# Optimization experiments

Measured on AMD Instinct MI355X. Metric: run time of the kernel, lower is better.

The kernel has to match this reference:

```python
import jax, jax.numpy as jnp
import numpy as np

NEG_INF = -1000000000.0
B, N, D, H, L, DFF = 4, 1024, 512, 8, 6, 2048
DH = D // H
R2 = 10.0 ** 2  # locality_radius^2
EPS = 1e-5


def setup_inputs() -> dict:
    key = jax.random.key(0)
    ks = jax.random.split(key, 16)
    s = 0.02
    inp = {
        "tokens": jax.random.normal(ks[0], (B, N, D), jnp.float32),
        "xy": jax.random.uniform(ks[1], (B, N, 2), jnp.float32) * 100.0,
        "Wq": jax.random.normal(ks[2], (L, D, D), jnp.float32) * s,
        "Wk": jax.random.normal(ks[3], (L, D, D), jnp.float32) * s,
        "Wv": jax.random.normal(ks[4], (L, D, D), jnp.float32) * s,
        "Wo": jax.random.normal(ks[5], (L, D, D), jnp.float32) * s,
        "bo": jnp.zeros((L, D), jnp.float32),
        "W1": jax.random.normal(ks[6], (L, D, DFF), jnp.float32) * s,
        "b1": jnp.zeros((L, DFF), jnp.float32),
        "W2": jax.random.normal(ks[7], (L, DFF, D), jnp.float32) * s,
        "b2": jnp.zeros((L, D), jnp.float32),
        "g1": jnp.ones((L, D), jnp.float32),
        "be1": jnp.zeros((L, D), jnp.float32),
        "g2": jnp.ones((L, D), jnp.float32),
        "be2": jnp.zeros((L, D), jnp.float32),
        "gf": jnp.ones((D,), jnp.float32),
        "bf": jnp.zeros((D,), jnp.float32),
        "alive": jax.random.randint(ks[8], (B, N), 0, 2, dtype=jnp.int32),
        "species": jax.random.randint(ks[9], (B, N), 0, 3, dtype=jnp.int32),
        "n_agents": 512,
    }
    return inp


def _ln(x, g, b):
    m = jnp.mean(x, axis=-1, keepdims=True)
    v = jnp.mean((x - m) ** 2, axis=-1, keepdims=True)
    return (x - m) * jax.lax.rsqrt(v + EPS) * g + b


def _build_bias(alive, xy, species, dtype):
    # (B,1,N,N) additive bias, broadcast over heads (original repeats per head)
    af = alive.astype(dtype)
    bias = (1.0 - af)[:, None, None, :] * NEG_INF  # dead keys
    d2 = jnp.sum((xy[:, :, None, :] - xy[:, None, :, :]) ** 2, axis=-1)  # (B,N,N)
    bias = bias + jnp.where(d2 > R2, NEG_INF, 0.0)[:, None, :, :]
    ia = species < 2
    ip = species == 2
    ct = (ia[:, :, None] & ip[:, None, :]) | (ip[:, :, None] & ia[:, None, :])
    bias = bias + jnp.where(ct, NEG_INF, 0.0)[:, None, :, :]
    return bias


def reference(tokens, xy, Wq, Wk, Wv, Wo, bo, W1, b1, W2, b2,
              g1, be1, g2, be2, gf, bf, alive, species, n_agents):
    bias = _build_bias(alive, xy, species, tokens.dtype)
    scale = np.float32(np.sqrt(DH))
    x = tokens
    for l in range(L):
        h = _ln(x, g1[l], be1[l])
        q = (h @ Wq[l]).reshape(B, N, H, DH)
        k = (h @ Wk[l]).reshape(B, N, H, DH)
        v = (h @ Wv[l]).reshape(B, N, H, DH)
        scores = jnp.einsum('bihd,bjhd->bhij', q, k) / scale + bias
        w = jax.nn.softmax(scores, axis=-1)
        o = jnp.einsum('bhij,bjhd->bihd', w, v).reshape(B, N, D)
        x = x + (o @ Wo[l] + bo[l])
        h2 = _ln(x, g2[l], be2[l])
        ff = jax.nn.gelu(h2 @ W1[l] + b1[l], approximate=False) @ W2[l] + b2[l]
        x = x + ff
    return _ln(x, gf, bf)
```

## Files before the change

kernel.cpp:

```cpp
#include <hip/hip_runtime.h>
#include <math.h>

namespace {

constexpr int B = 4, N = 1024, D = 512, H = 8, DHd = 64, L = 6, DFFd = 2048;
constexpr int M = B * N;
constexpr int QKVS = 3 * D;
constexpr float NEG = -1000000000.0f;
constexpr float R2c = 100.0f;

typedef __attribute__((ext_vector_type(8))) short bf16x8;
typedef __attribute__((ext_vector_type(4))) float f32x4;
typedef __attribute__((ext_vector_type(16))) float f32x16;

__device__ __forceinline__ short f2bf(float f) {
  union { float f; unsigned u; } c; c.f = f;
  unsigned r = (c.u + 0x7fffu + ((c.u >> 16) & 1u)) >> 16;
  return (short)r;
}

__device__ __forceinline__ float gelu_f(float x) {
  return 0.5f * x * (1.0f + erff(x * 0.70710678118654752f));
}

__global__ __launch_bounds__(256) void bias_kernel(
    const float* __restrict__ xy, const int* __restrict__ alive,
    const int* __restrict__ species, float* __restrict__ bias)
{
  int j = blockIdx.x * 256 + threadIdx.x;
  int i = blockIdx.y;
  int b = blockIdx.z;
  float xi = xy[((size_t)b * N + i) * 2 + 0];
  float yi = xy[((size_t)b * N + i) * 2 + 1];
  float xj = xy[((size_t)b * N + j) * 2 + 0];
  float yj = xy[((size_t)b * N + j) * 2 + 1];
  float dx = xi - xj, dy = yi - yj;
  float d2 = dx * dx + dy * dy;
  float bv = 0.0f;
  if (alive[b * N + j] == 0) bv += NEG;
  if (d2 > R2c) bv += NEG;
  int si = species[b * N + i], sj = species[b * N + j];
  bool ia = si < 2, ip = si == 2, ja = sj < 2, jp = sj == 2;
  if ((ia && jp) || (ip && ja)) bv += NEG;
  bias[((size_t)b * N + i) * N + j] = bv;
}

__global__ __launch_bounds__(256) void wprep_kernel(
    const float* __restrict__ src, short* __restrict__ dst,
    int K, int Nc, size_t srcLS, size_t dstLS)
{
  __shared__ float t[32][33];
  int k0 = blockIdx.x * 32, n0 = blockIdx.y * 32;
  src += (size_t)blockIdx.z * srcLS;
  dst += (size_t)blockIdx.z * dstLS;
  int r = threadIdx.x >> 5, c = threadIdx.x & 31;
#pragma unroll
  for (int i = 0; i < 4; ++i)
    t[r + i * 8][c] = src[(size_t)(k0 + r + i * 8) * Nc + n0 + c];
  __syncthreads();
#pragma unroll
  for (int i = 0; i < 4; ++i)
    dst[(size_t)(n0 + r + i * 8) * K + k0 + c] = f2bf(t[c][r + i * 8]);
}

__global__ __launch_bounds__(64) void ln_kernel(
    const float* __restrict__ x, const float* __restrict__ g,
    const float* __restrict__ be, float* __restrict__ outf,
    short* __restrict__ outb)
{
  int row = blockIdx.x;
  int tid = threadIdx.x;
  const float* xr = x + (size_t)row * D;
  float v[8];
  float sum = 0.f;
#pragma unroll
  for (int i = 0; i < 8; ++i) { v[i] = xr[tid + i * 64]; sum += v[i]; }
#pragma unroll
  for (int off = 32; off > 0; off >>= 1) sum += __shfl_down(sum, off);
  sum = __shfl(sum, 0);
  float mean = sum * (1.0f / D);
  float vs = 0.f;
#pragma unroll
  for (int i = 0; i < 8; ++i) { float d = v[i] - mean; vs += d * d; }
#pragma unroll
  for (int off = 32; off > 0; off >>= 1) vs += __shfl_down(vs, off);
  vs = __shfl(vs, 0);
  float rstd = rsqrtf(vs * (1.0f / D) + 1e-5f);
#pragma unroll
  for (int i = 0; i < 8; ++i) {
    int c = tid + i * 64;
    float o = (v[i] - mean) * rstd * g[c] + be[c];
    if (outb) outb[(size_t)row * D + c] = f2bf(o);
    else      outf[(size_t)row * D + c] = o;
  }
}

__global__ __launch_bounds__(256, 2) void gemm_sk_kernel(
    const short* __restrict__ A, const short* __restrict__ Bt,
    const float* __restrict__ bvec, float* __restrict__ Cf,
    short* __restrict__ Cb, int K, int Nc, int mode)
{
  __shared__ __align__(16) char smem[4 * 17408];
  const int bm = blockIdx.y * 64, bn = blockIdx.x * 64;
  const int t = threadIdx.x, wave = t >> 6, lane = t & 63;
  const int half = lane >> 5;
  const int l32 = lane & 31;
  const int srow4 = lane >> 2, sseg4 = lane & 3;

  char* slot = smem + wave * 17408;
  const int kw0 = wave * (K >> 2);
  const int nch = K >> 7;

  const short* Ab = A + (size_t)(bm + srow4) * K + kw0 + sseg4 * 8;
  const short* Bb = Bt + (size_t)(bn + srow4) * K + kw0 + sseg4 * 8;

  auto issue = [&](int p, int kc) {
    char* ab = slot + p * 8192;
    char* bb = slot + p * 8192 + 4096;
#pragma unroll
    for (int i = 0; i < 4; ++i) {
      __builtin_amdgcn_global_load_lds(
          (const __attribute__((address_space(1))) void*)(Ab + (size_t)i * 16 * K + kc),
          (__attribute__((address_space(3))) void*)(ab + i * 1024), 16, 0, 0);
    }
#pragma unroll
    for (int i = 0; i < 4; ++i) {
      __builtin_amdgcn_global_load_lds(
          (const __attribute__((address_space(1))) void*)(Bb + (size_t)i * 16 * K + kc),
          (__attribute__((address_space(3))) void*)(bb + i * 1024), 16, 0, 0);
    }
  };

  f32x16 acc[2][2];
#pragma unroll
  for (int i = 0; i < 2; ++i)
#pragma unroll
    for (int j = 0; j < 2; ++j)
#pragma unroll
      for (int r = 0; r < 16; ++r) acc[i][j][r] = 0.f;

  issue(0, 0);
  for (int c = 0; c < nch; ++c) {
    const int p = c & 1;
    if (c + 1 < nch) {
      issue(p ^ 1, (c + 1) * 32);
      asm volatile("s_waitcnt vmcnt(%0)" :: "i"(8) : "memory");
    } else {
      asm volatile("s_waitcnt vmcnt(0)" ::: "memory");
    }
    const short* As = (const short*)(slot + p * 8192);
    const short* Bs = (const short*)(slot + p * 8192 + 4096);
#pragma unroll
    for (int ks = 0; ks < 2; ++ks) {
      bf16x8 a0 = *(const bf16x8*)&As[(l32) * 32 + ks * 16 + half * 8];
      bf16x8 a1 = *(const bf16x8*)&As[(32 + l32) * 32 + ks * 16 + half * 8];
      bf16x8 b0 = *(const bf16x8*)&Bs[(l32) * 32 + ks * 16 + half * 8];
      bf16x8 b1 = *(const bf16x8*)&Bs[(32 + l32) * 32 + ks * 16 + half * 8];
      acc[0][0] = __builtin_amdgcn_mfma_f32_32x32x16_bf16(a0, b0, acc[0][0], 0, 0, 0);
      acc[0][1] = __builtin_amdgcn_mfma_f32_32x32x16_bf16(a0, b1, acc[0][1], 0, 0, 0);
      acc[1][0] = __builtin_amdgcn_mfma_f32_32x32x16_bf16(a1, b0, acc[1][0], 0, 0, 0);
      acc[1][1] = __builtin_amdgcn_mfma_f32_32x32x16_bf16(a1, b1, acc[1][1], 0, 0, 0);
    }
  }

  float* red = (float*)slot;
#pragma unroll
  for (int ti = 0; ti < 2; ++ti)
#pragma unroll
    for (int tj = 0; tj < 2; ++tj)
#pragma unroll
      for (int r = 0; r < 16; ++r) {
        int row = ti * 32 + (r & 3) + 8 * (r >> 2) + 4 * half;
        red[row * 68 + tj * 32 + l32] = acc[ti][tj][r];
      }
  __syncthreads();

  const int row = t >> 2, cs = (t & 3) * 16;
  const size_t orow = (size_t)(bm + row) * Nc + bn + cs;
#pragma unroll
  for (int u = 0; u < 4; ++u) {
    float4 s0 = *(const float4*)((const float*)(smem + 0 * 17408) + row * 68 + cs + u * 4);
    float4 s1 = *(const float4*)((const float*)(smem + 1 * 17408) + row * 68 + cs + u * 4);
    float4 s2 = *(const float4*)((const float*)(smem + 2 * 17408) + row * 68 + cs + u * 4);
    float4 s3 = *(const float4*)((const float*)(smem + 3 * 17408) + row * 68 + cs + u * 4);
    float o0 = s0.x + s1.x + s2.x + s3.x;
    float o1 = s0.y + s1.y + s2.y + s3.y;
    float o2 = s0.z + s1.z + s2.z + s3.z;
    float o3 = s0.w + s1.w + s2.w + s3.w;
    const int col = bn + cs + u * 4;
    if (mode == 0) {
      short4 w = {f2bf(o0), f2bf(o1), f2bf(o2), f2bf(o3)};
      *(short4*)&Cb[orow + u * 4] = w;
    } else if (mode == 1) {
      float4 bv = *(const float4*)&bvec[col];
      float4 rv = *(const float4*)&Cf[orow + u * 4];
      float4 w = {o0 + bv.x + rv.x, o1 + bv.y + rv.y, o2 + bv.z + rv.z, o3 + bv.w + rv.w};
      *(float4*)&Cf[orow + u * 4] = w;
    } else {
      float4 bv = *(const float4*)&bvec[col];
      short4 w = {f2bf(gelu_f(o0 + bv.x)), f2bf(gelu_f(o1 + bv.y)),
                  f2bf(gelu_f(o2 + bv.z)), f2bf(gelu_f(o3 + bv.w))};
      *(short4*)&Cb[orow + u * 4] = w;
    }
  }
}

__global__ __launch_bounds__(256) void attn_mfma_kernel(
    const short* __restrict__ qkv, const float* __restrict__ bias,
    short* __restrict__ o)
{
  constexpr int LDR = 72;
  __shared__ __align__(16) short Qs[64 * LDR];
  __shared__ __align__(16) short Ks[2][64 * LDR];
  __shared__ __align__(16) short Vt[2][64 * LDR];
  __shared__ __align__(16) short Ps[4 * 16 * LDR];

  const int q0 = blockIdx.x * 64;
  const int hh = blockIdx.y;
  const int b  = blockIdx.z;
  const int t  = threadIdx.x;
  const int wave = t >> 6;
  const int lane = t & 63;
  const int quad = lane >> 4;
  const int ln16 = lane & 15;
  const int srow = t >> 2, sseg = t & 3;

  {
    const short* qb = qkv + (size_t)(b * N + q0 + srow) * QKVS + hh * 64 + sseg * 16;
    *(bf16x8*)&Qs[srow * LDR + sseg * 16] = *(const bf16x8*)qb;
    *(bf16x8*)&Qs[srow * LDR + sseg * 16 + 8] = *(const bf16x8*)(qb + 8);
  }
  __syncthreads();

  const int qrow = wave * 16 + ln16;
  const bf16x8 qf0 = *(const bf16x8*)&Qs[qrow * LDR + quad * 8];
  const bf16x8 qf1 = *(const bf16x8*)&Qs[qrow * LDR + 32 + quad * 8];

  float m_run = -1e30f, l_run = 0.f;
  f32x4 Oacc[4];
#pragma unroll
  for (int dt = 0; dt < 4; ++dt) Oacc[dt] = (f32x4){0.f, 0.f, 0.f, 0.f};

  short* Psw = Ps + wave * 16 * LDR;
  const float* brow = bias + (size_t)(b * N + q0 + wave * 16 + ln16) * N;
  const short* kb0 = qkv + (size_t)b * N * QKVS + 512 + hh * 64 + sseg * 16;
  const short* vb0 = qkv + (size_t)b * N * QKVS + 1024 + hh * 64 + sseg * 16;

  bf16x8 k0r = *(const bf16x8*)(kb0 + (size_t)srow * QKVS);
  bf16x8 k1r = *(const bf16x8*)(kb0 + (size_t)srow * QKVS + 8);
  bf16x8 v0r = *(const bf16x8*)(vb0 + (size_t)srow * QKVS);
  bf16x8 v1r = *(const bf16x8*)(vb0 + (size_t)srow * QKVS + 8);
  float4 b4[4];
#pragma unroll
  for (int ks = 0; ks < 4; ++ks)
    b4[ks] = *(const float4*)&brow[ks * 16 + quad * 4];

  for (int kt = 0; kt < 16; ++kt) {
    const int p = kt & 1;
    *(bf16x8*)&Ks[p][srow * LDR + sseg * 16] = k0r;
    *(bf16x8*)&Ks[p][srow * LDR + sseg * 16 + 8] = k1r;
#pragma unroll
    for (int e = 0; e < 8; ++e) {
      Vt[p][(sseg * 16 + e) * LDR + srow] = v0r[e];
      Vt[p][(sseg * 16 + 8 + e) * LDR + srow] = v1r[e];
    }
    const int k0n = (kt + 1 < 16) ? (kt + 1) * 64 : 0;
    bf16x8 nk0 = *(const bf16x8*)(kb0 + (size_t)(k0n + srow) * QKVS);
    bf16x8 nk1 = *(const bf16x8*)(kb0 + (size_t)(k0n + srow) * QKVS + 8);
    bf16x8 nv0 = *(const bf16x8*)(vb0 + (size_t)(k0n + srow) * QKVS);
    bf16x8 nv1 = *(const bf16x8*)(vb0 + (size_t)(k0n + srow) * QKVS + 8);
    float4 bcur[4] = {b4[0], b4[1], b4[2], b4[3]};
#pragma unroll
    for (int ks = 0; ks < 4; ++ks)
      b4[ks] = *(const float4*)&brow[k0n + ks * 16 + quad * 4];
    asm volatile("s_waitcnt lgkmcnt(0)\n\ts_barrier" ::: "memory");

    float sv[4][4];
#pragma unroll
    for (int ks = 0; ks < 4; ++ks) {
      bf16x8 a0 = *(const bf16x8*)&Ks[p][(ks * 16 + ln16) * LDR + quad * 8];
      bf16x8 a1 = *(const bf16x8*)&Ks[p][(ks * 16 + ln16) * LDR + 32 + quad * 8];
      f32x4 z = (f32x4){0.f, 0.f, 0.f, 0.f};
      z = __builtin_amdgcn_mfma_f32_16x16x32_bf16(a0, qf0, z, 0, 0, 0);
      z = __builtin_amdgcn_mfma_f32_16x16x32_bf16(a1, qf1, z, 0, 0, 0);
#pragma unroll
      for (int r = 0; r < 4; ++r)
        sv[ks][r] = z[r] * 0.125f + (&bcur[ks].x)[r];
    }

    float mt = sv[0][0];
#pragma unroll
    for (int ks = 0; ks < 4; ++ks)
#pragma unroll
      for (int r = 0; r < 4; ++r) mt = fmaxf(mt, sv[ks][r]);
    mt = fmaxf(mt, __shfl_xor(mt, 16));
    mt = fmaxf(mt, __shfl_xor(mt, 32));
    const float m_new = fmaxf(m_run, mt);
    const float alpha = __expf(m_run - m_new);
    m_run = m_new;
    float rs = 0.f;
    float pv[4][4];
#pragma unroll
    for (int ks = 0; ks < 4; ++ks)
#pragma unroll
      for (int r = 0; r < 4; ++r) {
        float e = __expf(sv[ks][r] - m_new);
        pv[ks][r] = e;
        rs += e;
      }
    rs += __shfl_xor(rs, 16);
    rs += __shfl_xor(rs, 32);
    l_run = l_run * alpha + rs;
    float af[4];
#pragma unroll
    for (int r = 0; r < 4; ++r) af[r] = __shfl(alpha, quad * 4 + r);
#pragma unroll
    for (int dt = 0; dt < 4; ++dt)
#pragma unroll
      for (int r = 0; r < 4; ++r) Oacc[dt][r] *= af[r];

#pragma unroll
    for (int ks = 0; ks < 4; ++ks) {
      short4 pk = {f2bf(pv[ks][0]), f2bf(pv[ks][1]), f2bf(pv[ks][2]), f2bf(pv[ks][3])};
      *(short4*)&Psw[ln16 * LDR + ks * 16 + quad * 4] = pk;
    }

    bf16x8 ap0 = *(const bf16x8*)&Psw[ln16 * LDR + quad * 8];
    bf16x8 ap1 = *(const bf16x8*)&Psw[ln16 * LDR + 32 + quad * 8];
#pragma unroll
    for (int dt = 0; dt < 4; ++dt) {
      bf16x8 bv0 = *(const bf16x8*)&Vt[p][(dt * 16 + ln16) * LDR + quad * 8];
      bf16x8 bv1 = *(const bf16x8*)&Vt[p][(dt * 16 + ln16) * LDR + 32 + quad * 8];
      Oacc[dt] = __builtin_amdgcn_mfma_f32_16x16x32_bf16(ap0, bv0, Oacc[dt], 0, 0, 0);
      Oacc[dt] = __builtin_amdgcn_mfma_f32_16x16x32_bf16(ap1, bv1, Oacc[dt], 0, 0, 0);
    }

    k0r = nk0; k1r = nk1; v0r = nv0; v1r = nv1;
  }

  const float linv = 1.0f / l_run;
  float iv[4];
#pragma unroll
  for (int r = 0; r < 4; ++r) iv[r] = __shfl(linv, quad * 4 + r);
#pragma unroll
  for (int dt = 0; dt < 4; ++dt) {
#pragma unroll
    for (int r = 0; r < 4; ++r) {
      int row = q0 + wave * 16 + quad * 4 + r;
      o[(size_t)(b * N + row) * D + hh * 64 + dt * 16 + ln16] =
          f2bf(Oacc[dt][r] * iv[r]);
    }
  }
}

}

extern "C" void kernel_launch(void* const* d_in, const int* in_sizes, int n_in,
                              void* d_out, int out_size, void* d_ws, size_t ws_size,
                              hipStream_t stream)
{
  const float* tokens  = (const float*)d_in[0];
  const float* xy      = (const float*)d_in[1];
  const float* Wq      = (const float*)d_in[2];
  const float* Wk      = (const float*)d_in[3];
  const float* Wv      = (const float*)d_in[4];
  const float* Wo      = (const float*)d_in[5];
  const float* bo      = (const float*)d_in[6];
  const float* W1      = (const float*)d_in[7];
  const float* b1      = (const float*)d_in[8];
  const float* W2      = (const float*)d_in[9];
  const float* b2      = (const float*)d_in[10];
  const float* g1      = (const float*)d_in[11];
  const float* be1     = (const float*)d_in[12];
  const float* g2      = (const float*)d_in[13];
  const float* be2     = (const float*)d_in[14];
  const float* gf      = (const float*)d_in[15];
  const float* bf      = (const float*)d_in[16];
  const int*   alive   = (const int*)d_in[17];
  const int*   species = (const int*)d_in[18];

  char* p = (char*)d_ws;
  float* bias = (float*)p; p += (size_t)B * N * N * 4;
  float* x    = (float*)p; p += (size_t)M * D * 4;
  short* h    = (short*)p; p += (size_t)M * D * 2;
  short* qkv  = (short*)p; p += (size_t)M * DFFd * 2;
  short* ff   = qkv;
  short* Wqkvt = (short*)p; p += (size_t)L * QKVS * D * 2;
  short* Wot   = (short*)p; p += (size_t)L * D * D * 2;
  short* W1t   = (short*)p; p += (size_t)L * DFFd * D * 2;
  short* W2t   = (short*)p; p += (size_t)L * D * DFFd * 2;

  hipMemcpyAsync(x, tokens, sizeof(float) * (size_t)M * D,
                 hipMemcpyDeviceToDevice, stream);
  bias_kernel<<<dim3(N / 256, N, B), 256, 0, stream>>>(xy, alive, species, bias);

  wprep_kernel<<<dim3(16, 16, L), 256, 0, stream>>>(
      Wq, Wqkvt + (size_t)0 * D * D, D, D, (size_t)D * D, (size_t)QKVS * D);
  wprep_kernel<<<dim3(16, 16, L), 256, 0, stream>>>(
      Wk, Wqkvt + (size_t)1 * D * D, D, D, (size_t)D * D, (size_t)QKVS * D);
  wprep_kernel<<<dim3(16, 16, L), 256, 0, stream>>>(
      Wv, Wqkvt + (size_t)2 * D * D, D, D, (size_t)D * D, (size_t)QKVS * D);
  wprep_kernel<<<dim3(16, 16, L), 256, 0, stream>>>(
      Wo, Wot, D, D, (size_t)D * D, (size_t)D * D);
  wprep_kernel<<<dim3(16, 64, L), 256, 0, stream>>>(
      W1, W1t, D, DFFd, (size_t)D * DFFd, (size_t)DFFd * D);
  wprep_kernel<<<dim3(64, 16, L), 256, 0, stream>>>(
      W2, W2t, DFFd, D, (size_t)DFFd * D, (size_t)D * DFFd);

  for (int l = 0; l < L; ++l) {
    ln_kernel<<<M, 64, 0, stream>>>(x, g1 + l * D, be1 + l * D, nullptr, h);
    gemm_sk_kernel<<<dim3(QKVS / 64, M / 64), 256, 0, stream>>>(
        h, Wqkvt + (size_t)l * QKVS * D, nullptr, nullptr, qkv, D, QKVS, 0);
    attn_mfma_kernel<<<dim3(N / 64, H, B), 256, 0, stream>>>(qkv, bias, h);
    gemm_sk_kernel<<<dim3(D / 64, M / 64), 256, 0, stream>>>(
        h, Wot + (size_t)l * D * D, bo + l * D, x, nullptr, D, D, 1);
    ln_kernel<<<M, 64, 0, stream>>>(x, g2 + l * D, be2 + l * D, nullptr, h);
    gemm_sk_kernel<<<dim3(DFFd / 64, M / 64), 256, 0, stream>>>(
        h, W1t + (size_t)l * DFFd * D, b1 + l * DFFd, nullptr, ff, D, DFFd, 2);
    gemm_sk_kernel<<<dim3(D / 64, M / 64), 256, 0, stream>>>(
        ff, W2t + (size_t)l * D * DFFd, b2 + l * D, x, nullptr, DFFd, D, 1);
  }
  ln_kernel<<<M, 64, 0, stream>>>(x, gf, bf, (float*)d_out, nullptr);
}
```

Baseline: 994.4 us.

## Store attention bias as bf16 and deepen GEMM prefetch pipeline to four stages

The additive attention bias is now stored and read as bf16 instead of fp32, halving the bias traffic that every attention launch reads. The split-K GEMM now uses 16-wide K chunks in a four-slot ring, with three chunks in flight instead of double-buffered 32-wide chunks, aiming to hide more global-load latency. Bias values are exact multiples of -1e9, so bf16 rounding only perturbs huge negative numbers. The clamped tail prefetch re-issues redundant loads of the last chunk, and the smaller chunks mean more waitcnt points per MFMA.

```diff
diff --git a/kernel.cpp b/kernel.cpp
--- a/kernel.cpp
+++ b/kernel.cpp
@@ -19,13 +19,19 @@
   return (short)r;
 }
 
+__device__ __forceinline__ float bf2f(short s) {
+  union { unsigned u; float f; } c;
+  c.u = ((unsigned)(unsigned short)s) << 16;
+  return c.f;
+}
+
 __device__ __forceinline__ float gelu_f(float x) {
   return 0.5f * x * (1.0f + erff(x * 0.70710678118654752f));
 }
 
 __global__ __launch_bounds__(256) void bias_kernel(
     const float* __restrict__ xy, const int* __restrict__ alive,
-    const int* __restrict__ species, float* __restrict__ bias)
+    const int* __restrict__ species, short* __restrict__ bias)
 {
   int j = blockIdx.x * 256 + threadIdx.x;
   int i = blockIdx.y;
@@ -42,7 +48,7 @@
   int si = species[b * N + i], sj = species[b * N + j];
   bool ia = si < 2, ip = si == 2, ja = sj < 2, jp = sj == 2;
   if ((ia && jp) || (ip && ja)) bv += NEG;
-  bias[((size_t)b * N + i) * N + j] = bv;
+  bias[((size_t)b * N + i) * N + j] = f2bf(bv);
 }
 
 __global__ __launch_bounds__(256) void wprep_kernel(
@@ -105,29 +111,29 @@
   const int t = threadIdx.x, wave = t >> 6, lane = t & 63;
   const int half = lane >> 5;
   const int l32 = lane & 31;
-  const int srow4 = lane >> 2, sseg4 = lane & 3;
+  const int srow2 = lane >> 1, sseg2 = lane & 1;
 
   char* slot = smem + wave * 17408;
   const int kw0 = wave * (K >> 2);
-  const int nch = K >> 7;
-
-  const short* Ab = A + (size_t)(bm + srow4) * K + kw0 + sseg4 * 8;
-  const short* Bb = Bt + (size_t)(bn + srow4) * K + kw0 + sseg4 * 8;
-
-  auto issue = [&](int p, int kc) {
-    char* ab = slot + p * 8192;
-    char* bb = slot + p * 8192 + 4096;
-#pragma unroll
-    for (int i = 0; i < 4; ++i) {
+  const int nch = K >> 6;
+
+  const short* Ab = A + (size_t)(bm + srow2) * K + kw0 + sseg2 * 8;
+  const short* Bb = Bt + (size_t)(bn + srow2) * K + kw0 + sseg2 * 8;
+
+  auto issue = [&](int q, int c) {
+    char* ab = slot + q * 4096;
+    const int kc = c << 4;
+#pragma unroll
+    for (int i = 0; i < 2; ++i) {
       __builtin_amdgcn_global_load_lds(
-          (const __attribute__((address_space(1))) void*)(Ab + (size_t)i * 16 * K + kc),
+          (const __attribute__((address_space(1))) void*)(Ab + (size_t)i * 32 * K + kc),
           (__attribute__((address_space(3))) void*)(ab + i * 1024), 16, 0, 0);
     }
 #pragma unroll
-    for (int i = 0; i < 4; ++i) {
+    for (int i = 0; i < 2; ++i) {
       __builtin_amdgcn_global_load_lds(
-          (const __attribute__((address_space(1))) void*)(Bb + (size_t)i * 16 * K + kc),
-          (__attribute__((address_space(3))) void*)(bb + i * 1024), 16, 0, 0);
+          (const __attribute__((address_space(1))) void*)(Bb + (size_t)i * 32 * K + kc),
+          (__attribute__((address_space(3))) void*)(ab + 2048 + i * 1024), 16, 0, 0);
     }
   };
 
@@ -140,28 +146,25 @@
       for (int r = 0; r < 16; ++r) acc[i][j][r] = 0.f;
 
   issue(0, 0);
+  issue(1, 1);
+  issue(2, 2);
   for (int c = 0; c < nch; ++c) {
-    const int p = c & 1;
-    if (c + 1 < nch) {
-      issue(p ^ 1, (c + 1) * 32);
-      asm volatile("s_waitcnt vmcnt(%0)" :: "i"(8) : "memory");
-    } else {
-      asm volatile("s_waitcnt vmcnt(0)" ::: "memory");
-    }
-    const short* As = (const short*)(slot + p * 8192);
-    const short* Bs = (const short*)(slot + p * 8192 + 4096);
-#pragma unroll
-    for (int ks = 0; ks < 2; ++ks) {
-      bf16x8 a0 = *(const bf16x8*)&As[(l32) * 32 + ks * 16 + half * 8];
-      bf16x8 a1 = *(const bf16x8*)&As[(32 + l32) * 32 + ks * 16 + half * 8];
-      bf16x8 b0 = *(const bf16x8*)&Bs[(l32) * 32 + ks * 16 + half * 8];
-      bf16x8 b1 = *(const bf16x8*)&Bs[(32 + l32) * 32 + ks * 16 + half * 8];
-      acc[0][0] = __builtin_amdgcn_mfma_f32_32x32x16_bf16(a0, b0, acc[0][0], 0, 0, 0);
-      acc[0][1] = __builtin_amdgcn_mfma_f32_32x32x16_bf16(a0, b1, acc[0][1], 0, 0, 0);
-      acc[1][0] = __builtin_amdgcn_mfma_f32_32x32x16_bf16(a1, b0, acc[1][0], 0, 0, 0);
-      acc[1][1] = __builtin_amdgcn_mfma_f32_32x32x16_bf16(a1, b1, acc[1][1], 0, 0, 0);
-    }
-  }
+    const int q = c & 3;
+    const int cn = (c + 3 < nch) ? c + 3 : nch - 1;
+    issue((c + 3) & 3, cn);
+    asm volatile("s_waitcnt vmcnt(12)" ::: "memory");
+    const short* As = (const short*)(slot + q * 4096);
+    const short* Bs = (const short*)(slot + q * 4096 + 2048);
+    bf16x8 a0 = *(const bf16x8*)&As[(l32) * 16 + half * 8];
+    bf16x8 a1 = *(const bf16x8*)&As[(32 + l32) * 16 + half * 8];
+    bf16x8 b0 = *(const bf16x8*)&Bs[(l32) * 16 + half * 8];
+    bf16x8 b1 = *(const bf16x8*)&Bs[(32 + l32) * 16 + half * 8];
+    acc[0][0] = __builtin_amdgcn_mfma_f32_32x32x16_bf16(a0, b0, acc[0][0], 0, 0, 0);
+    acc[0][1] = __builtin_amdgcn_mfma_f32_32x32x16_bf16(a0, b1, acc[0][1], 0, 0, 0);
+    acc[1][0] = __builtin_amdgcn_mfma_f32_32x32x16_bf16(a1, b0, acc[1][0], 0, 0, 0);
+    acc[1][1] = __builtin_amdgcn_mfma_f32_32x32x16_bf16(a1, b1, acc[1][1], 0, 0, 0);
+  }
+  asm volatile("s_waitcnt vmcnt(0)" ::: "memory");
 
   float* red = (float*)slot;
 #pragma unroll
@@ -206,7 +209,7 @@
 }
 
 __global__ __launch_bounds__(256) void attn_mfma_kernel(
-    const short* __restrict__ qkv, const float* __restrict__ bias,
+    const short* __restrict__ qkv, const short* __restrict__ bias,
     short* __restrict__ o)
 {
   constexpr int LDR = 72;
@@ -242,9 +245,16 @@
   for (int dt = 0; dt < 4; ++dt) Oacc[dt] = (f32x4){0.f, 0.f, 0.f, 0.f};
 
   short* Psw = Ps + wave * 16 * LDR;
-  const float* brow = bias + (size_t)(b * N + q0 + wave * 16 + ln16) * N;
+  const short* brow = bias + (size_t)(b * N + q0 + wave * 16 + ln16) * N;
   const short* kb0 = qkv + (size_t)b * N * QKVS + 512 + hh * 64 + sseg * 16;
   const short* vb0 = qkv + (size_t)b * N * QKVS + 1024 + hh * 64 + sseg * 16;
+
+  auto ldb4 = [&](int off) -> float4 {
+    short4 s4 = *(const short4*)&brow[off];
+    float4 f;
+    f.x = bf2f(s4.x); f.y = bf2f(s4.y); f.z = bf2f(s4.z); f.w = bf2f(s4.w);
+    return f;
+  };
 
   bf16x8 k0r = *(const bf16x8*)(kb0 + (size_t)srow * QKVS);
   bf16x8 k1r = *(const bf16x8*)(kb0 + (size_t)srow * QKVS + 8);
@@ -253,7 +263,7 @@
   float4 b4[4];
 #pragma unroll
   for (int ks = 0; ks < 4; ++ks)
-    b4[ks] = *(const float4*)&brow[ks * 16 + quad * 4];
+    b4[ks] = ldb4(ks * 16 + quad * 4);
 
   for (int kt = 0; kt < 16; ++kt) {
     const int p = kt & 1;
@@ -272,7 +282,7 @@
     float4 bcur[4] = {b4[0], b4[1], b4[2], b4[3]};
 #pragma unroll
     for (int ks = 0; ks < 4; ++ks)
-      b4[ks] = *(const float4*)&brow[k0n + ks * 16 + quad * 4];
+      b4[ks] = ldb4(k0n + ks * 16 + quad * 4);
     asm volatile("s_waitcnt lgkmcnt(0)\n\ts_barrier" ::: "memory");
 
     float sv[4][4];
@@ -380,7 +390,7 @@
   const int*   species = (const int*)d_in[18];
 
   char* p = (char*)d_ws;
-  float* bias = (float*)p; p += (size_t)B * N * N * 4;
+  short* biasb = (short*)p; p += (size_t)B * N * N * 2;
   float* x    = (float*)p; p += (size_t)M * D * 4;
   short* h    = (short*)p; p += (size_t)M * D * 2;
   short* qkv  = (short*)p; p += (size_t)M * DFFd * 2;
@@ -392,7 +402,7 @@
 
   hipMemcpyAsync(x, tokens, sizeof(float) * (size_t)M * D,
                  hipMemcpyDeviceToDevice, stream);
-  bias_kernel<<<dim3(N / 256, N, B), 256, 0, stream>>>(xy, alive, species, bias);
+  bias_kernel<<<dim3(N / 256, N, B), 256, 0, stream>>>(xy, alive, species, biasb);
 
   wprep_kernel<<<dim3(16, 16, L), 256, 0, stream>>>(
       Wq, Wqkvt + (size_t)0 * D * D, D, D, (size_t)D * D, (size_t)QKVS * D);
@@ -411,7 +421,7 @@
     ln_kernel<<<M, 64, 0, stream>>>(x, g1 + l * D, be1 + l * D, nullptr, h);
     gemm_sk_kernel<<<dim3(QKVS / 64, M / 64), 256, 0, stream>>>(
         h, Wqkvt + (size_t)l * QKVS * D, nullptr, nullptr, qkv, D, QKVS, 0);
-    attn_mfma_kernel<<<dim3(N / 64, H, B), 256, 0, stream>>>(qkv, bias, h);
+    attn_mfma_kernel<<<dim3(N / 64, H, B), 256, 0, stream>>>(qkv, biasb, h);
     gemm_sk_kernel<<<dim3(D / 64, M / 64), 256, 0, stream>>>(
         h, Wot + (size_t)l * D * D, bo + l * D, x, nullptr, D, D, 1);
     ln_kernel<<<M, 64, 0, stream>>>(x, g2 + l * D, be2 + l * D, nullptr, h);
```

Result: slower. 1.355 ms (+36.3%).
